# Performance work log

Hardware: AMD Instinct MI355X
Metric: run time of the kernel (lower is better)

The kernel has to match this reference:

```python
import jax, jax.numpy as jnp
import numpy as np

B, T, C, H = 32, 512, 8, 256  # batch, seq_len, n_channels, HIDDEN_SIZE
G = 4 * H  # gate dim (i, f, g, o)


def setup_inputs() -> dict:
    key = jax.random.key(0)
    ks = jax.random.split(key, 12)
    k_scale = 1.0 / np.sqrt(H)  # PyTorch LSTM/Linear uniform init bound
    u = lambda k, shape: jax.random.uniform(k, shape, jnp.float32, -k_scale, k_scale)
    return {
        "x": jax.random.normal(ks[0], (B, T, C), jnp.float32),
        # per-channel LSTM layer 1 (input_size=1)
        "Wih1": u(ks[1], (C, G, 1)),
        "Whh1": u(ks[2], (C, G, H)),
        "bih1": u(ks[3], (C, G)),
        "bhh1": u(ks[4], (C, G)),
        # per-channel LSTM layer 2 (input_size=H)
        "Wih2": u(ks[5], (C, G, H)),
        "Whh2": u(ks[6], (C, G, H)),
        "bih2": u(ks[7], (C, G)),
        "bhh2": u(ks[8], (C, G)),
        # per-channel Linear(H, 1)
        "Wlin": u(ks[9], (C, H)),
        "blin": u(ks[10], (C,)),
    }


def _lstm_layer(x_proj, Whh):
    """x_proj: [T, C, B, 4H] precomputed input projection + biases.
    Whh: [C, 4H, H]. Returns hidden states [T, C, B, H]."""
    c_dim, b_dim = x_proj.shape[1], x_proj.shape[2]
    h0 = jnp.zeros((c_dim, b_dim, H), x_proj.dtype)
    c0 = jnp.zeros((c_dim, b_dim, H), x_proj.dtype)

    def step(carry, xp_t):
        h, c = carry
        gates = xp_t + jnp.einsum('cbh,cgh->cbg', h, Whh)
        i, f, g, o = jnp.split(gates, 4, axis=-1)  # PyTorch gate order i,f,g,o
        i = jax.nn.sigmoid(i)
        f = jax.nn.sigmoid(f)
        g = jnp.tanh(g)
        o = jax.nn.sigmoid(o)
        c_new = f * c + i * g
        h_new = o * jnp.tanh(c_new)
        return (h_new, c_new), h_new

    _, hs = jax.lax.scan(step, (h0, c0), x_proj)
    return hs  # [T, C, B, H]


def reference(x, Wih1, Whh1, bih1, bhh1, Wih2, Whh2, bih2, bhh2, Wlin, blin):
    # Dropout layers are identity in eval mode.
    # Layer 1: input_size=1 -> input projection is a per-channel scale of x.
    b1 = (bih1 + bhh1)[None, :, None, :]  # [1, C, 1, 4H]
    xp1 = jnp.einsum('btc,cg->tcbg', x, Wih1[:, :, 0]) + b1  # [T, C, B, 4H]
    h1 = _lstm_layer(xp1, Whh1)  # [T, C, B, H]

    # Layer 2
    b2 = (bih2 + bhh2)[None, :, None, :]
    xp2 = jnp.einsum('tcbh,cgh->tcbg', h1, Wih2) + b2
    h2 = _lstm_layer(xp2, Whh2)  # [T, C, B, H]

    # Per-channel Linear(H, 1), concatenated over channel dim.
    out = jnp.einsum('tcbh,ch->btc', h2, Wlin) + blin[None, None, :]
    return out  # [B, T, C]
```

## Files before the change

kernel.cpp:

```cpp
#include <hip/hip_runtime.h>

#define Bn 32
#define Tn 512
#define Cn 8
#define Hn 256
#define Gn 1024
#define NTHR 256
#define SLC  16
#define NBLK (Cn*2*SLC)
#define K2n  (Hn/2)
#define BUFS 4
#define EXU  (BUFS*Cn*K2n*Bn)
#define GP2  18

typedef __attribute__((ext_vector_type(8))) __bf16 bf16x8;
typedef __attribute__((ext_vector_type(8))) short  short8;
typedef __attribute__((ext_vector_type(4))) float  f32x4;
typedef __attribute__((ext_vector_type(4))) unsigned uintx4;
typedef unsigned long long u64;

__device__ __forceinline__ unsigned bfr(float f) {
    unsigned u = __float_as_uint(f);
    return (u + 0x7fffu + ((u >> 16) & 1u)) >> 16;
}
__device__ __forceinline__ float sigmf(float v)  { return 1.0f / (1.0f + __expf(-v)); }
__device__ __forceinline__ float tanh_f(float v) { return 1.0f - 2.0f / (__expf(2.0f * v) + 1.0f); }

__device__ __forceinline__ f32x4 mf(short8 a, short8 b, f32x4 c) {
    return __builtin_amdgcn_mfma_f32_16x16x32_bf16(
        __builtin_bit_cast(bf16x8, a), __builtin_bit_cast(bf16x8, b), c, 0, 0, 0);
}

__device__ __forceinline__ void splitw(const float* __restrict__ p, short8& hi, short8& lo) {
    short8 h, l;
#pragma unroll
    for (int j = 0; j < 8; ++j) {
        const float v = p[j];
        const unsigned hb = bfr(v);
        h[j] = (short)hb;
        l[j] = (short)bfr(v - __uint_as_float(hb << 16));
    }
    hi = h; lo = l;
}

__device__ __forceinline__ void ast64(u64* p, u64 v) {
    __hip_atomic_store(p, v, __ATOMIC_RELAXED, __HIP_MEMORY_SCOPE_AGENT);
}
__device__ __forceinline__ u64 ald64(const u64* p) {
    return __hip_atomic_load(p, __ATOMIC_RELAXED, __HIP_MEMORY_SCOPE_AGENT);
}

__global__ void __launch_bounds__(NTHR, 1)
lstm_mfma(const float* __restrict__ x,
          const float* __restrict__ Wih1, const float* __restrict__ Whh1,
          const float* __restrict__ bih1, const float* __restrict__ bhh1,
          const float* __restrict__ Wih2, const float* __restrict__ Whh2,
          const float* __restrict__ bih2, const float* __restrict__ bhh2,
          const float* __restrict__ Wlin, const float* __restrict__ blin,
          float* __restrict__ out, void* __restrict__ wsv, int use_part) {
    __shared__ float g1buf[2 * 64 * GP2];
    __shared__ float g2buf[2 * 64 * GP2];

    u64* EX1 = (u64*)wsv;
    u64* EX2 = EX1 + EXU;
    float* part = (float*)(EX2 + EXU);

    const int tid  = threadIdx.x;
    const int wg   = blockIdx.x;
    const int c    = wg & 7;
    const int s    = (wg >> 3) & 15;
    const int bh   = (wg >> 7) & 1;
    const int lane = tid & 63;
    const int wid  = tid >> 6;
    const int kg   = wid & 1;
    const int mh   = wid >> 1;
    const int n    = lane & 15;
    const int quad = lane >> 4;
    const int bn   = bh * 16 + n;

    short8 w1h[2][4], w1l[2][4], w2h[2][4], w2l[2][4], w3h[2][4], w3l[2][4];
#pragma unroll
    for (int mt = 0; mt < 2; ++mt) {
        const int r = mh * 32 + mt * 16 + n;
        const size_t g = (size_t)((r >> 4) * Hn + s * 16 + (r & 15));
        const size_t base = (size_t)c * Gn * Hn + g * Hn + kg * 128 + quad * 8;
#pragma unroll
        for (int kk = 0; kk < 4; ++kk) {
            splitw(Whh1 + base + kk * 32, w1h[mt][kk], w1l[mt][kk]);
            splitw(Wih2 + base + kk * 32, w2h[mt][kk], w2l[mt][kk]);
            splitw(Whh2 + base + kk * 32, w3h[mt][kk], w3l[mt][kk]);
        }
    }

    float wi1_r[2][4], bs1_r[2][4], bs2_r[2][4];
#pragma unroll
    for (int mt = 0; mt < 2; ++mt)
#pragma unroll
        for (int reg = 0; reg < 4; ++reg) {
            const int r = mh * 32 + mt * 16 + quad * 4 + reg;
            const int g = (r >> 4) * Hn + s * 16 + (r & 15);
            wi1_r[mt][reg] = Wih1[c * Gn + g];
            bs1_r[mt][reg] = bih1[c * Gn + g] + bhh1[c * Gn + g];
            bs2_r[mt][reg] = bih2[c * Gn + g] + bhh2[c * Gn + g];
        }

    const int jj = tid & 15;
    const int bb = tid >> 4;
    const int gb = bh * 16 + bb;
    const float wl = Wlin[c * Hn + s * 16 + jj];
    const float bl = blin[c];

    float c1 = 0.0f, c2 = 0.0f;

    for (int t = 0; t <= Tn; ++t) {
        const bool doA = (t < Tn);
        const bool doB = (t >= 1);
        const int wb = t & 3;
        const int rb = (t + 3) & 3;
        const unsigned ctag = (unsigned)(t % 3) + 1u;
        const unsigned ptag = (unsigned)((t + 2) % 3) + 1u;

        const float xv = doA ? x[(bn * Tn + t) * Cn + c] : 0.0f;

        const u64* E1 = EX1 + (size_t)(rb * Cn + c) * K2n * Bn;
        const u64* E2 = EX2 + (size_t)(rb * Cn + c) * K2n * Bn;
        const unsigned em = (ptag & 1u) | ((ptag & 2u) << 15);
        const bool chk1 = (t >= 1);
        const bool chk2 = (t >= 2);

        {
            const size_t poff = (size_t)(kg * 64 + lane) * Bn + bn;
            if (chk1 | chk2) {
                for (;;) {
                    unsigned bad = 0;
                    if (chk2) bad |= ((unsigned)(ald64(E2 + poff) >> 32) ^ em) & 0x00010001u;
                    if (chk1) bad |= ((unsigned)(ald64(E1 + poff) >> 32) ^ em) & 0x00010001u;
                    if (__all((int)(bad == 0))) break;
                    __builtin_amdgcn_s_sleep(1);
                }
            }
        }

        short8 f2h[4], f2l[4], f1h[4], f1l[4];
        bool got1 = false, got2 = false;
        for (;;) {
            unsigned bad1 = 0, bad2 = 0;
            if (!got2) {
#pragma unroll
                for (int kk = 0; kk < 4; ++kk) {
                    uintx4 a2h, a2l;
#pragma unroll
                    for (int j2 = 0; j2 < 4; ++j2) {
                        const int k2 = kg * 64 + kk * 16 + quad * 4 + j2;
                        const u64 v2 = ald64(E2 + k2 * Bn + bn);
                        a2h[j2] = (unsigned)v2;
                        a2l[j2] = (unsigned)(v2 >> 32);
                        bad2 |= (a2l[j2] ^ em) & 0x00010001u;
                    }
                    f2h[kk] = __builtin_bit_cast(short8, a2h);
                    f2l[kk] = __builtin_bit_cast(short8, a2l);
                }
            }
            if (!got1) {
#pragma unroll
                for (int kk = 0; kk < 4; ++kk) {
                    uintx4 a1h, a1l;
#pragma unroll
                    for (int j2 = 0; j2 < 4; ++j2) {
                        const int k2 = kg * 64 + kk * 16 + quad * 4 + j2;
                        const u64 v1 = ald64(E1 + k2 * Bn + bn);
                        a1h[j2] = (unsigned)v1;
                        a1l[j2] = (unsigned)(v1 >> 32);
                        bad1 |= (a1l[j2] ^ em) & 0x00010001u;
                    }
                    f1h[kk] = __builtin_bit_cast(short8, a1h);
                    f1l[kk] = __builtin_bit_cast(short8, a1l);
                }
            }
            if (!got2) got2 = !chk2 || __all((int)(bad2 == 0));
            if (!got1) got1 = !chk1 || __all((int)(bad1 == 0));
            if (got1 && got2) break;
            __builtin_amdgcn_s_sleep(1);
        }

        f32x4 a1a[2] = {{0,0,0,0},{0,0,0,0}}, a1x[2] = {{0,0,0,0},{0,0,0,0}};
        f32x4 a2a[2] = {{0,0,0,0},{0,0,0,0}}, a2x[2] = {{0,0,0,0},{0,0,0,0}};
#pragma unroll
        for (int kk = 0; kk < 4; ++kk)
#pragma unroll
            for (int mt = 0; mt < 2; ++mt) {
                a2a[mt] = mf(w3h[mt][kk], f2h[kk], a2a[mt]);
                a2x[mt] = mf(w3l[mt][kk], f2h[kk], mf(w3h[mt][kk], f2l[kk], a2x[mt]));
                a1a[mt] = mf(w1h[mt][kk], f1h[kk], a1a[mt]);
                a1x[mt] = mf(w1l[mt][kk], f1h[kk], mf(w1h[mt][kk], f1l[kk], a1x[mt]));
                a2a[mt] = mf(w2h[mt][kk], f1h[kk], a2a[mt]);
                a2x[mt] = mf(w2l[mt][kk], f1h[kk], mf(w2h[mt][kk], f1l[kk], a2x[mt]));
            }

#pragma unroll
        for (int mt = 0; mt < 2; ++mt)
#pragma unroll
            for (int reg = 0; reg < 4; ++reg) {
                const int r = mh * 32 + mt * 16 + quad * 4 + reg;
                const int off = (kg * 64 + r) * GP2 + n;
                float e1 = a1a[mt][reg] + a1x[mt][reg];
                float e2 = a2a[mt][reg] + a2x[mt][reg];
                if (kg == 0) {
                    e1 += xv * wi1_r[mt][reg] + bs1_r[mt][reg];
                    e2 += bs2_r[mt][reg];
                }
                g1buf[off] = e1;
                g2buf[off] = e2;
            }
        __syncthreads();

        const unsigned cm = (ctag & 1u) | ((ctag & 2u) << 15);

        if (doA) {
            const float iv = sigmf (g1buf[jj * GP2 + bb]        + g1buf[(64 + jj) * GP2 + bb]);
            const float fv = sigmf (g1buf[(16 + jj) * GP2 + bb] + g1buf[(80 + jj) * GP2 + bb]);
            const float gv = tanh_f(g1buf[(32 + jj) * GP2 + bb] + g1buf[(96 + jj) * GP2 + bb]);
            const float ov = sigmf (g1buf[(48 + jj) * GP2 + bb] + g1buf[(112 + jj) * GP2 + bb]);
            c1 = fv * c1 + iv * gv;
            const float h1v = ov * tanh_f(c1);
            const unsigned hb = bfr(h1v);
            const unsigned lb = bfr(h1v - __uint_as_float(hb << 16));
            const unsigned packed = (hb << 16) | lb;
            const unsigned nbp = (unsigned)__shfl_xor((int)packed, 1, 64);
            if ((jj & 1) == 0) {
                const unsigned hip = (packed >> 16) | (nbp & 0xffff0000u);
                unsigned lop = (packed & 0xffffu) | (nbp << 16);
                lop = (lop & 0xFFFEFFFEu) | cm;
                const int k2 = s * 8 + (jj >> 1);
                ast64(EX1 + (size_t)(wb * Cn + c) * K2n * Bn + k2 * Bn + gb,
                      (u64)hip | ((u64)lop << 32));
            }
        }
        if (doB) {
            const float iv = sigmf (g2buf[jj * GP2 + bb]        + g2buf[(64 + jj) * GP2 + bb]);
            const float fv = sigmf (g2buf[(16 + jj) * GP2 + bb] + g2buf[(80 + jj) * GP2 + bb]);
            const float gv = tanh_f(g2buf[(32 + jj) * GP2 + bb] + g2buf[(96 + jj) * GP2 + bb]);
            const float ov = sigmf (g2buf[(48 + jj) * GP2 + bb] + g2buf[(112 + jj) * GP2 + bb]);
            c2 = fv * c2 + iv * gv;
            const float h2v = ov * tanh_f(c2);
            if (t < Tn) {
                const unsigned hb = bfr(h2v);
                const unsigned lb = bfr(h2v - __uint_as_float(hb << 16));
                const unsigned packed = (hb << 16) | lb;
                const unsigned nbp = (unsigned)__shfl_xor((int)packed, 1, 64);
                if ((jj & 1) == 0) {
                    const unsigned hip = (packed >> 16) | (nbp & 0xffff0000u);
                    unsigned lop = (packed & 0xffffu) | (nbp << 16);
                    lop = (lop & 0xFFFEFFFEu) | cm;
                    const int k2 = s * 8 + (jj >> 1);
                    ast64(EX2 + (size_t)(wb * Cn + c) * K2n * Bn + k2 * Bn + gb,
                          (u64)hip | ((u64)lop << 32));
                }
            } else {
                (void)__shfl_xor(0, 1, 64);
            }

            float pv = h2v * wl;
            pv += __shfl_xor(pv, 1, 64);
            pv += __shfl_xor(pv, 2, 64);
            pv += __shfl_xor(pv, 4, 64);
            pv += __shfl_xor(pv, 8, 64);
            if (jj == 0) {
                if (use_part) {
                    part[(((t - 1) * Cn + c) * SLC + s) * Bn + gb] = pv;
                } else {
                    atomicAdd(&out[(gb * Tn + (t - 1)) * Cn + c], pv + (s == 0 ? bl : 0.0f));
                }
            }
        }

        __syncthreads();
    }
}

__global__ void reduce_out(const float* __restrict__ part, const float* __restrict__ blin,
                           float* __restrict__ out) {
    const int t = blockIdx.x;
    const int c = threadIdx.x >> 5;
    const int b = threadIdx.x & 31;
    float v = blin[c];
#pragma unroll
    for (int s = 0; s < SLC; ++s) v += part[((t * Cn + c) * SLC + s) * Bn + b];
    out[(b * Tn + t) * Cn + c] = v;
}

extern "C" void kernel_launch(void* const* d_in, const int* in_sizes, int n_in,
                              void* d_out, int out_size, void* d_ws, size_t ws_size,
                              hipStream_t stream) {
    const float* x    = (const float*)d_in[0];
    const float* Wih1 = (const float*)d_in[1];
    const float* Whh1 = (const float*)d_in[2];
    const float* bih1 = (const float*)d_in[3];
    const float* bhh1 = (const float*)d_in[4];
    const float* Wih2 = (const float*)d_in[5];
    const float* Whh2 = (const float*)d_in[6];
    const float* bih2 = (const float*)d_in[7];
    const float* bhh2 = (const float*)d_in[8];
    const float* Wlin = (const float*)d_in[9];
    const float* blin = (const float*)d_in[10];
    float* out = (float*)d_out;

    const size_t h_bytes    = (size_t)2 * EXU * sizeof(u64);
    const size_t part_bytes = (size_t)Tn * Cn * SLC * Bn * sizeof(float);
    const int use_part = (ws_size >= h_bytes + part_bytes) ? 1 : 0;

    hipMemsetAsync(d_ws, 0, h_bytes, stream);
    if (!use_part)
        hipMemsetAsync(d_out, 0, (size_t)out_size * sizeof(float), stream);

    lstm_mfma<<<NBLK, NTHR, 0, stream>>>(
        x, Wih1, Whh1, bih1, bhh1, Wih2, Whh2, bih2, bhh2, Wlin, blin, out, d_ws, use_part);

    if (use_part) {
        const float* part = (const float*)((const char*)d_ws + h_bytes);
        reduce_out<<<Tn, Cn * Bn, 0, stream>>>(part, blin, out);
    }
}
```

Measured before the change: 2.114 ms.

## Split exchange waits per layer and publish layer-2 hidden state first

Drops the separate pre-poll spin on both exchange buffers. Each step now waits for the layer-2 buffer alone and runs its matmul contribution, then waits for the layer-1 buffer and runs the remaining MFMAs, so compute overlaps the arrival of the other buffer. The layer-2 cell update and its global publish are moved ahead of layer-1, so the older dependency is released to other blocks sooner. Removing the cheap pre-poll may cause more full-fragment reloads while spinning.

```diff
diff --git a/kernel.cpp b/kernel.cpp
--- a/kernel.cpp
+++ b/kernel.cpp
@@ -128,74 +128,69 @@
         const bool chk1 = (t >= 1);
         const bool chk2 = (t >= 2);
 
+        f32x4 a2a[2] = {{0,0,0,0},{0,0,0,0}}, a2x[2] = {{0,0,0,0},{0,0,0,0}};
         {
-            const size_t poff = (size_t)(kg * 64 + lane) * Bn + bn;
-            if (chk1 | chk2) {
-                for (;;) {
-                    unsigned bad = 0;
-                    if (chk2) bad |= ((unsigned)(ald64(E2 + poff) >> 32) ^ em) & 0x00010001u;
-                    if (chk1) bad |= ((unsigned)(ald64(E1 + poff) >> 32) ^ em) & 0x00010001u;
-                    if (__all((int)(bad == 0))) break;
-                    __builtin_amdgcn_s_sleep(1);
-                }
-            }
-        }
-
-        short8 f2h[4], f2l[4], f1h[4], f1l[4];
-        bool got1 = false, got2 = false;
-        for (;;) {
-            unsigned bad1 = 0, bad2 = 0;
-            if (!got2) {
+            short8 f2h[4], f2l[4];
+            for (;;) {
+                unsigned bad = 0;
 #pragma unroll
                 for (int kk = 0; kk < 4; ++kk) {
-                    uintx4 a2h, a2l;
+                    uintx4 ah, al;
 #pragma unroll
                     for (int j2 = 0; j2 < 4; ++j2) {
                         const int k2 = kg * 64 + kk * 16 + quad * 4 + j2;
                         const u64 v2 = ald64(E2 + k2 * Bn + bn);
-                        a2h[j2] = (unsigned)v2;
-                        a2l[j2] = (unsigned)(v2 >> 32);
-                        bad2 |= (a2l[j2] ^ em) & 0x00010001u;
+                        ah[j2] = (unsigned)v2;
+                        al[j2] = (unsigned)(v2 >> 32);
+                        bad |= (al[j2] ^ em) & 0x00010001u;
                     }
-                    f2h[kk] = __builtin_bit_cast(short8, a2h);
-                    f2l[kk] = __builtin_bit_cast(short8, a2l);
-                }
-            }
-            if (!got1) {
+                    f2h[kk] = __builtin_bit_cast(short8, ah);
+                    f2l[kk] = __builtin_bit_cast(short8, al);
+                }
+                if (!chk2 || __all((int)(bad == 0))) break;
+                __builtin_amdgcn_s_sleep(1);
+            }
+#pragma unroll
+            for (int kk = 0; kk < 4; ++kk)
+#pragma unroll
+                for (int mt = 0; mt < 2; ++mt) {
+                    a2a[mt] = mf(w3h[mt][kk], f2h[kk], a2a[mt]);
+                    a2x[mt] = mf(w3l[mt][kk], f2h[kk], mf(w3h[mt][kk], f2l[kk], a2x[mt]));
+                }
+        }
+
+        f32x4 a1a[2] = {{0,0,0,0},{0,0,0,0}}, a1x[2] = {{0,0,0,0},{0,0,0,0}};
+        {
+            short8 f1h[4], f1l[4];
+            for (;;) {
+                unsigned bad = 0;
 #pragma unroll
                 for (int kk = 0; kk < 4; ++kk) {
-                    uintx4 a1h, a1l;
+                    uintx4 ah, al;
 #pragma unroll
                     for (int j2 = 0; j2 < 4; ++j2) {
                         const int k2 = kg * 64 + kk * 16 + quad * 4 + j2;
                         const u64 v1 = ald64(E1 + k2 * Bn + bn);
-                        a1h[j2] = (unsigned)v1;
-                        a1l[j2] = (unsigned)(v1 >> 32);
-                        bad1 |= (a1l[j2] ^ em) & 0x00010001u;
+                        ah[j2] = (unsigned)v1;
+                        al[j2] = (unsigned)(v1 >> 32);
+                        bad |= (al[j2] ^ em) & 0x00010001u;
                     }
-                    f1h[kk] = __builtin_bit_cast(short8, a1h);
-                    f1l[kk] = __builtin_bit_cast(short8, a1l);
-                }
-            }
-            if (!got2) got2 = !chk2 || __all((int)(bad2 == 0));
-            if (!got1) got1 = !chk1 || __all((int)(bad1 == 0));
-            if (got1 && got2) break;
-            __builtin_amdgcn_s_sleep(1);
-        }
-
-        f32x4 a1a[2] = {{0,0,0,0},{0,0,0,0}}, a1x[2] = {{0,0,0,0},{0,0,0,0}};
-        f32x4 a2a[2] = {{0,0,0,0},{0,0,0,0}}, a2x[2] = {{0,0,0,0},{0,0,0,0}};
-#pragma unroll
-        for (int kk = 0; kk < 4; ++kk)
-#pragma unroll
-            for (int mt = 0; mt < 2; ++mt) {
-                a2a[mt] = mf(w3h[mt][kk], f2h[kk], a2a[mt]);
-                a2x[mt] = mf(w3l[mt][kk], f2h[kk], mf(w3h[mt][kk], f2l[kk], a2x[mt]));
-                a1a[mt] = mf(w1h[mt][kk], f1h[kk], a1a[mt]);
-                a1x[mt] = mf(w1l[mt][kk], f1h[kk], mf(w1h[mt][kk], f1l[kk], a1x[mt]));
-                a2a[mt] = mf(w2h[mt][kk], f1h[kk], a2a[mt]);
-                a2x[mt] = mf(w2l[mt][kk], f1h[kk], mf(w2h[mt][kk], f1l[kk], a2x[mt]));
-            }
+                    f1h[kk] = __builtin_bit_cast(short8, ah);
+                    f1l[kk] = __builtin_bit_cast(short8, al);
+                }
+                if (!chk1 || __all((int)(bad == 0))) break;
+                __builtin_amdgcn_s_sleep(1);
+            }
+#pragma unroll
+            for (int kk = 0; kk < 4; ++kk)
+#pragma unroll
+                for (int mt = 0; mt < 2; ++mt) {
+                    a1a[mt] = mf(w1h[mt][kk], f1h[kk], a1a[mt]);
+                    a1x[mt] = mf(w1l[mt][kk], f1h[kk], mf(w1h[mt][kk], f1l[kk], a1x[mt]));
+                    a2a[mt] = mf(w2h[mt][kk], f1h[kk], a2a[mt]);
+                    a2x[mt] = mf(w2l[mt][kk], f1h[kk], mf(w2h[mt][kk], f1l[kk], a2x[mt]));
+                }
+        }
 
 #pragma unroll
         for (int mt = 0; mt < 2; ++mt)
@@ -215,6 +210,32 @@
         __syncthreads();
 
         const unsigned cm = (ctag & 1u) | ((ctag & 2u) << 15);
+
+        float h2v = 0.0f;
+        if (doB) {
+            const float iv = sigmf (g2buf[jj * GP2 + bb]        + g2buf[(64 + jj) * GP2 + bb]);
+            const float fv = sigmf (g2buf[(16 + jj) * GP2 + bb] + g2buf[(80 + jj) * GP2 + bb]);
+            const float gv = tanh_f(g2buf[(32 + jj) * GP2 + bb] + g2buf[(96 + jj) * GP2 + bb]);
+            const float ov = sigmf (g2buf[(48 + jj) * GP2 + bb] + g2buf[(112 + jj) * GP2 + bb]);
+            c2 = fv * c2 + iv * gv;
+            h2v = ov * tanh_f(c2);
+            if (t < Tn) {
+                const unsigned hb = bfr(h2v);
+                const unsigned lb = bfr(h2v - __uint_as_float(hb << 16));
+                const unsigned packed = (hb << 16) | lb;
+                const unsigned nbp = (unsigned)__shfl_xor((int)packed, 1, 64);
+                if ((jj & 1) == 0) {
+                    const unsigned hip = (packed >> 16) | (nbp & 0xffff0000u);
+                    unsigned lop = (packed & 0xffffu) | (nbp << 16);
+                    lop = (lop & 0xFFFEFFFEu) | cm;
+                    const int k2 = s * 8 + (jj >> 1);
+                    ast64(EX2 + (size_t)(wb * Cn + c) * K2n * Bn + k2 * Bn + gb,
+                          (u64)hip | ((u64)lop << 32));
+                }
+            } else {
+                (void)__shfl_xor(0, 1, 64);
+            }
+        }
 
         if (doA) {
             const float iv = sigmf (g1buf[jj * GP2 + bb]        + g1buf[(64 + jj) * GP2 + bb]);
@@ -236,30 +257,8 @@
                       (u64)hip | ((u64)lop << 32));
             }
         }
+
         if (doB) {
-            const float iv = sigmf (g2buf[jj * GP2 + bb]        + g2buf[(64 + jj) * GP2 + bb]);
-            const float fv = sigmf (g2buf[(16 + jj) * GP2 + bb] + g2buf[(80 + jj) * GP2 + bb]);
-            const float gv = tanh_f(g2buf[(32 + jj) * GP2 + bb] + g2buf[(96 + jj) * GP2 + bb]);
-            const float ov = sigmf (g2buf[(48 + jj) * GP2 + bb] + g2buf[(112 + jj) * GP2 + bb]);
-            c2 = fv * c2 + iv * gv;
-            const float h2v = ov * tanh_f(c2);
-            if (t < Tn) {
-                const unsigned hb = bfr(h2v);
-                const unsigned lb = bfr(h2v - __uint_as_float(hb << 16));
-                const unsigned packed = (hb << 16) | lb;
-                const unsigned nbp = (unsigned)__shfl_xor((int)packed, 1, 64);
-                if ((jj & 1) == 0) {
-                    const unsigned hip = (packed >> 16) | (nbp & 0xffff0000u);
-                    unsigned lop = (packed & 0xffffu) | (nbp << 16);
-                    lop = (lop & 0xFFFEFFFEu) | cm;
-                    const int k2 = s * 8 + (jj >> 1);
-                    ast64(EX2 + (size_t)(wb * Cn + c) * K2n * Bn + k2 * Bn + gb,
-                          (u64)hip | ((u64)lop << 32));
-                }
-            } else {
-                (void)__shfl_xor(0, 1, 64);
-            }
-
             float pv = h2v * wl;
             pv += __shfl_xor(pv, 1, 64);
             pv += __shfl_xor(pv, 2, 64);
```

Result: faster. 1.787 ms (-15.5%).
